# Optimization experiments

Hardware: AMD Instinct MI355X
Metric: run time of the kernel (lower is better)

## Reference

```python
import jax, jax.numpy as jnp
import numpy as np

DIM = 1024
DIM_HEADS = 128   # dim_inner
HEADS = 8         # dim_out // dim_heads
DHEAD = DIM_HEADS // HEADS  # = 16, per the Rearrange '(qkv h d)'
EPS = 1e-6


def setup_inputs() -> dict:
    key = jax.random.key(0)
    k1, k2, k3 = jax.random.split(key, 3)
    x = jax.random.normal(k1, (8, 4096, DIM), dtype=jnp.float32)
    norm_weight = jnp.ones((DIM,), dtype=jnp.float32)
    w_qkv = jax.random.normal(k2, (3 * DIM_HEADS, DIM), dtype=jnp.float32) * (1.0 / np.sqrt(DIM))
    temperature = jnp.zeros((HEADS, 1, 1), dtype=jnp.float32)
    w_out = jax.random.normal(k3, (DIM, DIM_HEADS), dtype=jnp.float32) * (1.0 / np.sqrt(DIM_HEADS))
    return {"x": x, "norm_weight": norm_weight, "w_qkv": w_qkv,
            "temperature": temperature, "w_out": w_out}


def _l2norm(t, axis=-1):
    # F.normalize(p=2): divide by max(||t||, eps) with eps=1e-12
    n = jnp.sqrt(jnp.sum(t * t, axis=axis, keepdims=True))
    return t / jnp.maximum(n, 1e-12)


def reference(x, norm_weight, w_qkv, temperature, w_out):
    b, n, _ = x.shape
    # RMSNorm
    ms = jnp.mean(x * x, axis=-1, keepdims=True)
    xn = x * jax.lax.rsqrt(ms + EPS) * norm_weight
    # QKV projection: b n (3 h d) -> 3 b h d n
    qkv = jnp.einsum('bnc,oc->bno', xn, w_qkv)
    qkv = qkv.reshape(b, n, 3, HEADS, DHEAD).transpose(2, 0, 3, 4, 1)  # [3,b,h,d,n]
    q, k, v = qkv[0], qkv[1], qkv[2]
    # l2-normalize along token axis (last axis, n)
    q = _l2norm(q)
    k = _l2norm(k)
    q = q * jnp.exp(temperature)  # (h,1,1) broadcasts over (b,h,d,n)
    # XCiT channel (cross-covariance) attention: d x d similarity over tokens
    sim = jnp.einsum('bhin,bhjn->bhij', q, k)
    attn = jax.nn.softmax(sim, axis=-1)
    out = jnp.einsum('bhij,bhjn->bhin', attn, v)  # [b,h,d,n]
    # b h d n -> b n (h d), then output projection
    out = out.transpose(0, 3, 1, 2).reshape(b, n, HEADS * DHEAD)
    return jnp.einsum('bnc,oc->bno', out, w_out)
```

## Files before the change

### kernel.cpp

```cpp
#include <hip/hip_runtime.h>
#include <hip/hip_bf16.h>
#include <stdint.h>

typedef __bf16 bf16_t;
typedef __bf16 bf16x4 __attribute__((ext_vector_type(4)));
typedef __bf16 bf16x8 __attribute__((ext_vector_type(8)));
typedef float  f32x4  __attribute__((ext_vector_type(4)));

#define DIM    1024
#define NTOK   4096
#define NB     8
#define ROWS   (NB*NTOK)
#define QKVC   384
#define INNER  128

#define GLD16(g, l) __builtin_amdgcn_global_load_lds( \
    (const __attribute__((address_space(1))) void*)(g), \
    (__attribute__((address_space(3))) void*)(l), 16, 0, 0)

#define OFF_WQ    131072u
#define OFF_QKV   1048576u
#define OFF_STATS 26214400u
#define OFF_ATTN  30932992u
#define OFF_WEFF  30998528u

__global__ __launch_bounds__(256) void k_wconv(const float* __restrict__ wq,
    const float* __restrict__ nw, bf16_t* __restrict__ wqb)
{
    int o = blockIdx.x;
    int c = threadIdx.x * 4;
    float4 wv = *reinterpret_cast<const float4*>(wq + (size_t)o*DIM + c);
    float4 nv = *reinterpret_cast<const float4*>(nw + c);
    bf16_t* dst = wqb + (size_t)o*DIM + c;
    dst[0]=(bf16_t)(wv.x*nv.x); dst[1]=(bf16_t)(wv.y*nv.y);
    dst[2]=(bf16_t)(wv.z*nv.z); dst[3]=(bf16_t)(wv.w*nv.w);
}

__global__ __launch_bounds__(512, 2) void k_qkv_gemm(const float* __restrict__ x,
    const bf16_t* __restrict__ wqb, bf16_t* __restrict__ qkv)
{
    __shared__ bf16_t Al[2][128*64];
    __shared__ bf16_t Bl[2][384*64];
    __shared__ float srow[128];
    int mt = blockIdx.x;
    int row0 = mt*128;
    int t = threadIdx.x;
    int lane = t & 63, lr = lane & 15, lg = lane >> 4;
    int w = t >> 6, wm = w >> 2, wn = w & 3;

    int rA = t >> 2;
    int fo = (t & 3) * 16;
    const float* xrow = x + (size_t)(row0 + rA)*DIM + fo;
    int ws0 = ((t & 3)*2)     ^ (rA & 7);
    int ws1 = ((t & 3)*2 + 1) ^ (rA & 7);

    int srB = t >> 3;
    int sk8 = ((t & 7) ^ (srB & 7)) * 8;
    const bf16_t* bbase = wqb + (size_t)srB*DIM + sk8;
    int ldsoff = (t & ~63) * 8;

    int rsw = lr & 7;

    float4 u0, u1, u2, u3;

#define LOADA(kt) do {                                                   \
        const float4* _xs = reinterpret_cast<const float4*>(xrow + (kt)*64); \
        u0 = _xs[0]; u1 = _xs[1]; u2 = _xs[2]; u3 = _xs[3];              \
    } while (0)

#define STAGEB(buf, kt) do {                                             \
        int _ko = (kt)*64;                                               \
        _Pragma("unroll")                                                \
        for (int _c = 0; _c < 6; _c++)                                   \
            GLD16(bbase + _ko + (size_t)(64*_c)*DIM,                     \
                  &Bl[buf][ldsoff + _c*4096]);                           \
    } while (0)

#define WRITEA(buf) do {                                                 \
        ssq += u0.x*u0.x + u0.y*u0.y + u0.z*u0.z + u0.w*u0.w             \
             + u1.x*u1.x + u1.y*u1.y + u1.z*u1.z + u1.w*u1.w             \
             + u2.x*u2.x + u2.y*u2.y + u2.z*u2.z + u2.w*u2.w             \
             + u3.x*u3.x + u3.y*u3.y + u3.z*u3.z + u3.w*u3.w;            \
        bf16x8 v0, v1;                                                   \
        v0[0]=(bf16_t)u0.x; v0[1]=(bf16_t)u0.y; v0[2]=(bf16_t)u0.z;      \
        v0[3]=(bf16_t)u0.w; v0[4]=(bf16_t)u1.x; v0[5]=(bf16_t)u1.y;      \
        v0[6]=(bf16_t)u1.z; v0[7]=(bf16_t)u1.w;                          \
        v1[0]=(bf16_t)u2.x; v1[1]=(bf16_t)u2.y; v1[2]=(bf16_t)u2.z;      \
        v1[3]=(bf16_t)u2.w; v1[4]=(bf16_t)u3.x; v1[5]=(bf16_t)u3.y;      \
        v1[6]=(bf16_t)u3.z; v1[7]=(bf16_t)u3.w;                          \
        *reinterpret_cast<bf16x8*>(&Al[buf][rA*64 + ws0*8]) = v0;        \
        *reinterpret_cast<bf16x8*>(&Al[buf][rA*64 + ws1*8]) = v1;        \
    } while (0)

    float ssq = 0.f;
    f32x4 acc[4][6] = {};

    LOADA(0);
    STAGEB(0, 0);
    WRITEA(0);
    __syncthreads();

    for (int kt = 0; kt < 16; kt++) {
        int cur = kt & 1;
        if (kt < 15) {
            LOADA(kt + 1);
            STAGEB(cur ^ 1, kt + 1);
        }
        #pragma unroll
        for (int kk = 0; kk < 2; kk++) {
            int kb = ((kk*4 + lg) ^ rsw) * 8;
            bf16x8 af[4], bfr[6];
            #pragma unroll
            for (int mi = 0; mi < 4; mi++)
                af[mi] = *reinterpret_cast<const bf16x8*>(
                    &Al[cur][(wm*64 + mi*16 + lr)*64 + kb]);
            #pragma unroll
            for (int ni = 0; ni < 6; ni++)
                bfr[ni] = *reinterpret_cast<const bf16x8*>(
                    &Bl[cur][(wn*96 + ni*16 + lr)*64 + kb]);
            #pragma unroll
            for (int mi = 0; mi < 4; mi++)
                #pragma unroll
                for (int ni = 0; ni < 6; ni++)
                    acc[mi][ni] = __builtin_amdgcn_mfma_f32_16x16x32_bf16(
                        af[mi], bfr[ni], acc[mi][ni], 0, 0, 0);
        }
        if (kt < 15) WRITEA(cur ^ 1);
        __syncthreads();
    }
#undef LOADA
#undef STAGEB
#undef WRITEA

    ssq += __shfl_xor(ssq, 1, 64);
    ssq += __shfl_xor(ssq, 2, 64);
    if ((t & 3) == 0) srow[rA] = rsqrtf(ssq*(1.0f/DIM) + 1e-6f);
    __syncthreads();

    #pragma unroll
    for (int mi = 0; mi < 4; mi++)
        #pragma unroll
        for (int ni = 0; ni < 6; ni++) {
            int col_g = wn*96 + ni*16 + lr;
            #pragma unroll
            for (int rr = 0; rr < 4; rr++) {
                int rloc = wm*64 + mi*16 + lg*4 + rr;
                qkv[(size_t)(row0 + rloc)*QKVC + col_g] =
                    (bf16_t)(acc[mi][ni][rr] * srow[rloc]);
            }
        }
}

__global__ __launch_bounds__(256) void k_stats(const bf16_t* __restrict__ qkv,
    float* __restrict__ stats)
{
    __shared__ bf16_t qk[64*264];
    int bid = blockIdx.x;
    int b = bid >> 6, ch = bid & 63;
    int t = threadIdx.x;
    #pragma unroll
    for (int rd = 0; rd < 8; rd++) {
        int tok = (t >> 5) + 8*rd;
        int c8  = (t & 31) * 8;
        *reinterpret_cast<uint4*>(&qk[tok*264 + c8]) =
            *reinterpret_cast<const uint4*>(
                qkv + ((size_t)b*NTOK + ch*64 + tok)*QKVC + c8);
    }
    __syncthreads();
    int h = t >> 5, s = t & 31, i0 = (s >> 4)*8, j = s & 15;
    float gram[8] = {}, qsq[8] = {}, ksq = 0.f;
    for (int tok = 0; tok < 64; tok++) {
        bf16x8 q8 = *reinterpret_cast<const bf16x8*>(&qk[tok*264 + h*16 + i0]);
        float kf = (float)qk[tok*264 + 128 + h*16 + j];
        ksq += kf*kf;
        #pragma unroll
        for (int m = 0; m < 8; m++) {
            float qf = (float)q8[m];
            gram[m] += qf*kf;
            qsq[m]  += qf*qf;
        }
    }
    float* base = stats + ((size_t)(b*64 + ch)*8 + h)*288;
    #pragma unroll
    for (int m = 0; m < 8; m++) base[(i0 + m)*16 + j] = gram[m];
    if (j == 0) {
        #pragma unroll
        for (int m = 0; m < 8; m++) base[256 + i0 + m] = qsq[m];
    }
    if (s < 16) base[272 + j] = ksq;
}

__global__ __launch_bounds__(256) void k_attn(const float* __restrict__ stats,
    const float* __restrict__ temp, float* __restrict__ attn)
{
    int bid = blockIdx.x;
    int b = bid >> 3, h = bid & 7;
    int t = threadIdx.x, i = t >> 4, j = t & 15;
    float gsum = 0.f, qs = 0.f, ks = 0.f;
    for (int ch = 0; ch < 64; ch++) {
        const float* base = stats + ((size_t)(b*64 + ch)*8 + h)*288;
        gsum += base[i*16 + j];
        qs   += base[256 + i];
        ks   += base[272 + j];
    }
    float et  = expf(temp[h]);
    float sim = gsum * et / (fmaxf(sqrtf(qs), 1e-12f) * fmaxf(sqrtf(ks), 1e-12f));
    float m = sim;
    #pragma unroll
    for (int d = 1; d < 16; d <<= 1) m = fmaxf(m, __shfl_xor(m, d, 16));
    float e = expf(sim - m);
    float ssum = e;
    #pragma unroll
    for (int d = 1; d < 16; d <<= 1) ssum += __shfl_xor(ssum, d, 16);
    attn[((size_t)(b*8 + h)*16 + i)*16 + j] = e / ssum;
}

__global__ __launch_bounds__(256) void k_weff(const float* __restrict__ attn,
    const float* __restrict__ wout, bf16_t* __restrict__ weff)
{
    __shared__ float at[2048];
    int bid = blockIdx.x;
    int b = bid >> 5, ob = (bid & 31)*32;
    int t = threadIdx.x;
    #pragma unroll
    for (int r = 0; r < 8; r++) at[t + 256*r] = attn[(size_t)b*2048 + t + 256*r];
    __syncthreads();
    int c = t & 127, h = c >> 4, j = c & 15, oo = (t >> 7)*16;
    #pragma unroll
    for (int m = 0; m < 16; m++) {
        int o = ob + oo + m;
        float acc = 0.f;
        #pragma unroll
        for (int i2 = 0; i2 < 16; i2++)
            acc += wout[(size_t)o*INNER + h*16 + i2] * at[(h*16 + i2)*16 + j];
        weff[((size_t)b*DIM + o)*INNER + c] = (bf16_t)acc;
    }
}

__global__ __launch_bounds__(256) void k_out_gemm(const bf16_t* __restrict__ qkv,
    const bf16_t* __restrict__ weff, float* __restrict__ out)
{
    __shared__ bf16_t Al[128*136];
    __shared__ bf16_t Bl[128*136];
    int bid = blockIdx.x;
    int b = bid >> 8, rem = bid & 255;
    int mt = rem >> 3, nt = rem & 7;
    int tok0 = mt*128, o0 = nt*128;
    int t = threadIdx.x;
    #pragma unroll
    for (int rd = 0; rd < 8; rd++) {
        int r  = (t >> 4) + 16*rd;
        int c8 = (t & 15) * 8;
        *reinterpret_cast<uint4*>(&Al[r*136 + c8]) =
            *reinterpret_cast<const uint4*>(
                qkv + ((size_t)b*NTOK + tok0 + r)*QKVC + 256 + c8);
        *reinterpret_cast<uint4*>(&Bl[r*136 + c8]) =
            *reinterpret_cast<const uint4*>(
                weff + ((size_t)b*DIM + o0 + r)*INNER + c8);
    }
    __syncthreads();
    int w = t >> 6, lane = t & 63, lr = lane & 15, lg = lane >> 4;
    int wr = (w & 1)*64, wc = (w >> 1)*64;
    f32x4 acc[4][4] = {};
    #pragma unroll
    for (int kk = 0; kk < 4; kk++) {
        int kb = kk*32 + lg*8;
        bf16x8 af[4], bfr[4];
        #pragma unroll
        for (int mi = 0; mi < 4; mi++)
            af[mi] = *reinterpret_cast<const bf16x8*>(&Al[(wr + mi*16 + lr)*136 + kb]);
        #pragma unroll
        for (int ni = 0; ni < 4; ni++)
            bfr[ni] = *reinterpret_cast<const bf16x8*>(&Bl[(wc + ni*16 + lr)*136 + kb]);
        #pragma unroll
        for (int mi = 0; mi < 4; mi++)
            #pragma unroll
            for (int ni = 0; ni < 4; ni++)
                acc[mi][ni] = __builtin_amdgcn_mfma_f32_16x16x32_bf16(
                    af[mi], bfr[ni], acc[mi][ni], 0, 0, 0);
    }
    #pragma unroll
    for (int mi = 0; mi < 4; mi++)
        #pragma unroll
        for (int ni = 0; ni < 4; ni++) {
            int col_g = o0 + wc + ni*16 + lr;
            #pragma unroll
            for (int r = 0; r < 4; r++) {
                int row_g = tok0 + wr + mi*16 + lg*4 + r;
                out[((size_t)b*NTOK + row_g)*DIM + col_g] = acc[mi][ni][r];
            }
        }
}

extern "C" void kernel_launch(void* const* d_in, const int* in_sizes, int n_in,
                              void* d_out, int out_size, void* d_ws, size_t ws_size,
                              hipStream_t stream)
{
    const float* x    = (const float*)d_in[0];
    const float* nw   = (const float*)d_in[1];
    const float* wq   = (const float*)d_in[2];
    const float* temp = (const float*)d_in[3];
    const float* wout = (const float*)d_in[4];
    float* out = (float*)d_out;

    char* ws = (char*)d_ws;
    bf16_t* wqb   = (bf16_t*)(ws + OFF_WQ);
    bf16_t* qkv   = (bf16_t*)(ws + OFF_QKV);
    float*  stats = (float*)(ws + OFF_STATS);
    float*  attn  = (float*)(ws + OFF_ATTN);
    bf16_t* weff  = (bf16_t*)(ws + OFF_WEFF);

    k_wconv    <<<384,  256, 0, stream>>>(wq, nw, wqb);
    k_qkv_gemm <<<256,  512, 0, stream>>>(x, wqb, qkv);
    k_stats    <<<512,  256, 0, stream>>>(qkv, stats);
    k_attn     <<<64,   256, 0, stream>>>(stats, temp, attn);
    k_weff     <<<256,  256, 0, stream>>>(attn, wout, weff);
    k_out_gemm <<<2048, 256, 0, stream>>>(qkv, weff, out);
}
```

Baseline: 123.4 us.

## Fuse q/k Gram statistics into QKV GEMM epilogue using LDS and MFMA

The separate stats kernel is removed. The QKV GEMM now stages its q and k output tiles in shared memory, writes only v to global memory, and computes per-head q·k Gram partials with MFMA plus squared norms directly from LDS. This avoids one kernel launch, the global write of q/k, and the reread of q/k by the stats pass. In exchange the GEMM epilogue gets longer, its LDS reads are strided, and k_attn now reduces over 32 chunks of 128 tokens instead of 64 chunks of 64.

```diff
diff --git a/kernel.cpp b/kernel.cpp
--- a/kernel.cpp
+++ b/kernel.cpp
@@ -3,7 +3,6 @@
 #include <stdint.h>
 
 typedef __bf16 bf16_t;
-typedef __bf16 bf16x4 __attribute__((ext_vector_type(4)));
 typedef __bf16 bf16x8 __attribute__((ext_vector_type(8)));
 typedef float  f32x4  __attribute__((ext_vector_type(4)));
 
@@ -37,7 +36,8 @@
 }
 
 __global__ __launch_bounds__(512, 2) void k_qkv_gemm(const float* __restrict__ x,
-    const bf16_t* __restrict__ wqb, bf16_t* __restrict__ qkv)
+    const bf16_t* __restrict__ wqb, bf16_t* __restrict__ qkv,
+    float* __restrict__ stats)
 {
     __shared__ bf16_t Al[2][128*64];
     __shared__ bf16_t Bl[2][384*64];
@@ -137,6 +137,7 @@
     if ((t & 3) == 0) srow[rA] = rsqrtf(ssq*(1.0f/DIM) + 1e-6f);
     __syncthreads();
 
+    bf16_t* qk = &Bl[0][0];
     #pragma unroll
     for (int mi = 0; mi < 4; mi++)
         #pragma unroll
@@ -145,49 +146,45 @@
             #pragma unroll
             for (int rr = 0; rr < 4; rr++) {
                 int rloc = wm*64 + mi*16 + lg*4 + rr;
-                qkv[(size_t)(row0 + rloc)*QKVC + col_g] =
-                    (bf16_t)(acc[mi][ni][rr] * srow[rloc]);
+                bf16_t val = (bf16_t)(acc[mi][ni][rr] * srow[rloc]);
+                if (wn*96 + ni*16 >= 256)
+                    qkv[(size_t)(row0 + rloc)*QKVC + col_g] = val;
+                else
+                    qk[rloc*256 + col_g] = val;
             }
         }
-}
-
-__global__ __launch_bounds__(256) void k_stats(const bf16_t* __restrict__ qkv,
-    float* __restrict__ stats)
-{
-    __shared__ bf16_t qk[64*264];
-    int bid = blockIdx.x;
-    int b = bid >> 6, ch = bid & 63;
-    int t = threadIdx.x;
-    #pragma unroll
-    for (int rd = 0; rd < 8; rd++) {
-        int tok = (t >> 5) + 8*rd;
-        int c8  = (t & 31) * 8;
-        *reinterpret_cast<uint4*>(&qk[tok*264 + c8]) =
-            *reinterpret_cast<const uint4*>(
-                qkv + ((size_t)b*NTOK + ch*64 + tok)*QKVC + c8);
-    }
-    __syncthreads();
-    int h = t >> 5, s = t & 31, i0 = (s >> 4)*8, j = s & 15;
-    float gram[8] = {}, qsq[8] = {}, ksq = 0.f;
-    for (int tok = 0; tok < 64; tok++) {
-        bf16x8 q8 = *reinterpret_cast<const bf16x8*>(&qk[tok*264 + h*16 + i0]);
-        float kf = (float)qk[tok*264 + 128 + h*16 + j];
-        ksq += kf*kf;
-        #pragma unroll
-        for (int m = 0; m < 8; m++) {
-            float qf = (float)q8[m];
-            gram[m] += qf*kf;
-            qsq[m]  += qf*qf;
-        }
-    }
-    float* base = stats + ((size_t)(b*64 + ch)*8 + h)*288;
-    #pragma unroll
-    for (int m = 0; m < 8; m++) base[(i0 + m)*16 + j] = gram[m];
-    if (j == 0) {
-        #pragma unroll
-        for (int m = 0; m < 8; m++) base[256 + i0 + m] = qsq[m];
-    }
-    if (s < 16) base[272 + j] = ksq;
+    __syncthreads();
+
+    {
+        int h = w;
+        f32x4 g = {};
+        #pragma unroll
+        for (int ks = 0; ks < 4; ks++) {
+            bf16x8 afr, bfr2;
+            #pragma unroll
+            for (int e = 0; e < 8; e++) {
+                int tt = ks*32 + lg*8 + e;
+                afr[e]  = qk[tt*256 + h*16 + lr];
+                bfr2[e] = qk[tt*256 + 128 + h*16 + lr];
+            }
+            g = __builtin_amdgcn_mfma_f32_16x16x32_bf16(afr, bfr2, g, 0, 0, 0);
+        }
+        float* base = stats + ((size_t)mt*8 + h)*288;
+        #pragma unroll
+        for (int reg = 0; reg < 4; reg++)
+            base[(lg*4 + reg)*16 + lr] = g[reg];
+        float qs = 0.f, ks2 = 0.f;
+        #pragma unroll
+        for (int e = 0; e < 32; e++) {
+            int tt = lg*32 + e;
+            float qv = (float)qk[tt*256 + h*16 + lr];
+            float kv = (float)qk[tt*256 + 128 + h*16 + lr];
+            qs += qv*qv; ks2 += kv*kv;
+        }
+        qs  += __shfl_xor(qs, 16, 64);  qs  += __shfl_xor(qs, 32, 64);
+        ks2 += __shfl_xor(ks2, 16, 64); ks2 += __shfl_xor(ks2, 32, 64);
+        if (lane < 16) { base[256 + lr] = qs; base[272 + lr] = ks2; }
+    }
 }
 
 __global__ __launch_bounds__(256) void k_attn(const float* __restrict__ stats,
@@ -197,8 +194,8 @@
     int b = bid >> 3, h = bid & 7;
     int t = threadIdx.x, i = t >> 4, j = t & 15;
     float gsum = 0.f, qs = 0.f, ks = 0.f;
-    for (int ch = 0; ch < 64; ch++) {
-        const float* base = stats + ((size_t)(b*64 + ch)*8 + h)*288;
+    for (int ch = 0; ch < 32; ch++) {
+        const float* base = stats + ((size_t)(b*32 + ch)*8 + h)*288;
         gsum += base[i*16 + j];
         qs   += base[256 + i];
         ks   += base[272 + j];
@@ -311,8 +308,7 @@
     bf16_t* weff  = (bf16_t*)(ws + OFF_WEFF);
 
     k_wconv    <<<384,  256, 0, stream>>>(wq, nw, wqb);
-    k_qkv_gemm <<<256,  512, 0, stream>>>(x, wqb, qkv);
-    k_stats    <<<512,  256, 0, stream>>>(qkv, stats);
+    k_qkv_gemm <<<256,  512, 0, stream>>>(x, wqb, qkv, stats);
     k_attn     <<<64,   256, 0, stream>>>(stats, temp, attn);
     k_weff     <<<256,  256, 0, stream>>>(attn, wout, weff);
     k_out_gemm <<<2048, 256, 0, stream>>>(qkv, weff, out);
```

Result: faster. 102.0 us, median of 2 (-17.3%).
